# Optimization experiments

Measured on AMD Instinct MI355X. Metric: run time of the kernel, lower is better.

Reference implementation:

```python
import math
import jax, jax.numpy as jnp
import numpy as np

D_MODEL = 768
N_HEADS = 12


def setup_inputs() -> dict:
    key = jax.random.key(0)
    kx, kw, kb = jax.random.split(key, 3)
    x = jax.random.normal(kx, (2, 2048, D_MODEL), dtype=jnp.float32)
    # nn.Linear(D, 3D): weight [3D, D], bias [3D]; init ~ U(-1/sqrt(D), 1/sqrt(D))
    bound = 1.0 / math.sqrt(D_MODEL)
    W_kqv = jax.random.uniform(kw, (3 * D_MODEL, D_MODEL), dtype=jnp.float32, minval=-bound, maxval=bound)
    b_kqv = jax.random.uniform(kb, (3 * D_MODEL,), dtype=jnp.float32, minval=-bound, maxval=bound)
    return {"x": x, "W_kqv": W_kqv, "b_kqv": b_kqv}


def reference(x, W_kqv, b_kqv):
    N, C, D = x.shape
    H = N_HEADS
    hd = D // H
    z = jnp.einsum('ncd,ed->nce', x, W_kqv) + b_kqv  # [N, C, 3D]
    # order in source: k first, then q, then v
    k = z[:, :, :D].reshape(N, C, H, hd).transpose(0, 2, 1, 3)       # [N,H,C,hd]
    q = z[:, :, D:2 * D].reshape(N, C, H, hd).transpose(0, 2, 1, 3)
    v = z[:, :, 2 * D:].reshape(N, C, H, hd).transpose(0, 2, 1, 3)
    # NOTE: faithful to source: scale by sqrt(D) (full model dim), not sqrt(head_dim)
    scores = jnp.einsum('nhqd,nhkd->nhqk', q, k) / math.sqrt(D)
    causal = jnp.tril(jnp.ones((C, C), dtype=bool))
    scores = jnp.where(causal, scores, -jnp.inf)
    attn = jax.nn.softmax(scores, axis=-1)
    out = jnp.einsum('nhqk,nhkd->nhqd', attn, v)  # [N,H,C,hd]
    return out.transpose(0, 2, 1, 3).reshape(N, C, D)
```

## Files before the change

### kernel.cpp

```cpp
#include <hip/hip_runtime.h>
#include <stdint.h>

#define D_MODEL 768
#define E3      2304
#define NCTX    2048
#define NH      12
#define HD      64
#define MROWS   4096
#define NHTOT   24

typedef __attribute__((ext_vector_type(8))) short short8;
typedef __attribute__((ext_vector_type(4))) short bf16x4;
typedef __attribute__((ext_vector_type(4))) float f32x4;

typedef __attribute__((address_space(3))) uint32_t lds_u32;
typedef __attribute__((address_space(1))) uint32_t glob_u32;

__device__ __forceinline__ void async_copy16(const void* g, void* l) {
    __builtin_amdgcn_global_load_lds((const glob_u32*)(uintptr_t)g,
                                     (lds_u32*)(uint32_t)(uintptr_t)l, 16, 0, 0);
}

__device__ __forceinline__ unsigned short f2bf(float f) {
    uint32_t u = __builtin_bit_cast(uint32_t, f);
    u += 0x7fffu + ((u >> 16) & 1u);
    return (unsigned short)(u >> 16);
}

__device__ __forceinline__ float fast_exp2(float x) {
#if __has_builtin(__builtin_amdgcn_exp2f)
    return __builtin_amdgcn_exp2f(x);
#else
    return __expf(x * 0.6931471805599453f);
#endif
}

#if __has_builtin(__builtin_amdgcn_mfma_f32_16x16x16bf16_1k)
#define HAVE_MFMA16 1
#else
#define HAVE_MFMA16 0
#endif

__global__ void cast_bf16_kernel(const float* __restrict__ in, unsigned short* __restrict__ out) {
    int i = blockIdx.x * blockDim.x + threadIdx.x;
    float4 v = ((const float4*)in)[i];
    ushort4 o;
    o.x = f2bf(v.x); o.y = f2bf(v.y); o.z = f2bf(v.z); o.w = f2bf(v.w);
    ((ushort4*)out)[i] = o;
}

__global__ __launch_bounds__(256) void qkv_gemm(const unsigned short* __restrict__ A,
                                                const unsigned short* __restrict__ B,
                                                const float* __restrict__ bias,
                                                unsigned short* __restrict__ Zq,
                                                unsigned short* __restrict__ Kb,
                                                unsigned short* __restrict__ Vb) {
    __shared__ __attribute__((aligned(16))) unsigned short sA[128 * 64];
    __shared__ __attribute__((aligned(16))) unsigned short sB[128 * 64];

    const int tid  = threadIdx.x;
    const int wave = tid >> 6;
    const int lane = tid & 63;
    const int quad = lane >> 4;
    const int l15  = lane & 15;
    const int wm   = (wave >> 1) << 6;
    const int wn   = (wave & 1) << 6;
    const int row0 = blockIdx.y * 128;
    const int col0 = blockIdx.x * 128;

    const int srow   = lane >> 3;
    const int schunk = (lane & 7) * 8;

    f32x4 acc[4][4] = {};

    for (int k0 = 0; k0 < D_MODEL; k0 += 64) {
        __syncthreads();
#pragma unroll
        for (int c = 0; c < 4; ++c) {
            const int rbase = wave * 32 + c * 8;
            async_copy16(A + (size_t)(row0 + rbase + srow) * D_MODEL + k0 + schunk, &sA[rbase * 64]);
            async_copy16(B + (size_t)(col0 + rbase + srow) * D_MODEL + k0 + schunk, &sB[rbase * 64]);
        }
        __syncthreads();

#pragma unroll
        for (int ks = 0; ks < 2; ++ks) {
            short8 aF[4], bF[4];
#pragma unroll
            for (int i = 0; i < 4; ++i)
                aF[i] = *(const short8*)&sA[(wm + i * 16 + l15) * 64 + ks * 32 + quad * 8];
#pragma unroll
            for (int i = 0; i < 4; ++i)
                bF[i] = *(const short8*)&sB[(wn + i * 16 + l15) * 64 + ks * 32 + quad * 8];
#pragma unroll
            for (int i = 0; i < 4; ++i)
#pragma unroll
                for (int j = 0; j < 4; ++j)
                    acc[i][j] = __builtin_amdgcn_mfma_f32_16x16x32_bf16(aF[i], bF[j], acc[i][j], 0, 0, 0);
        }
    }

    if (col0 < D_MODEL) {
#pragma unroll
        for (int j = 0; j < 4; ++j) {
            const int col = col0 + wn + j * 16 + l15;
            const float bv = bias[col];
            const int h = col >> 6, d = col & 63;
            const int ks = d >> 5, quadd = (d >> 3) & 3, e = d & 7;
#pragma unroll
            for (int i = 0; i < 4; ++i) {
                const int row = row0 + wm + i * 16 + quad * 4;
                const int n = row >> 11;
                const int key = row & (NCTX - 1);
                const int kb = key >> 6;
                const int ct = i;
                const size_t base = ((size_t)((n * NH + h) * 32 + kb)) * 4096
                                  + (((ks * 4 + ct) * 4 + quadd) * 16) * 8 + e;
#pragma unroll
                for (int r = 0; r < 4; ++r)
                    Kb[base + (size_t)(quad * 4 + r) * 8] = f2bf(acc[i][j][r] + bv);
            }
        }
    } else if (col0 < 2 * D_MODEL) {
        const float zscale = 0.036084391824351615f * 1.4426950408889634f;
#pragma unroll
        for (int j = 0; j < 4; ++j) {
            const int col = col0 - D_MODEL + wn + j * 16 + l15;
            const float bv = bias[col0 + wn + j * 16 + l15];
#pragma unroll
            for (int i = 0; i < 4; ++i) {
                const int row = row0 + wm + i * 16 + quad * 4;
#pragma unroll
                for (int r = 0; r < 4; ++r)
                    Zq[(size_t)(row + r) * D_MODEL + col] = f2bf((acc[i][j][r] + bv) * zscale);
            }
        }
    } else {
#pragma unroll
        for (int j = 0; j < 4; ++j) {
            const int col = col0 + wn + j * 16 + l15;
            const float bv = bias[col];
            const int ch = col - 2 * D_MODEL;
            const int h = ch >> 6, d = ch & 63;
            const int dt = d >> 4, l15d = d & 15;
#pragma unroll
            for (int i = 0; i < 4; ++i) {
                const int row = row0 + wm + i * 16 + quad * 4;
                const int n = row >> 11;
                const int key = row & (NCTX - 1);
                const int kb = key >> 6;
                const int ct = i, quadv = quad;
                ushort4 w4;
                w4.x = f2bf(acc[i][j][0] + bv);
                w4.y = f2bf(acc[i][j][1] + bv);
                w4.z = f2bf(acc[i][j][2] + bv);
                w4.w = f2bf(acc[i][j][3] + bv);
                *(ushort4*)&Vb[((size_t)((n * NH + h) * 32 + kb)) * 4096
                               + (((ct * 4 + dt) * 4 + quadv) * 16 + l15d) * 4] = w4;
            }
        }
    }
}

__global__ __launch_bounds__(256) void attn_kernel(const unsigned short* __restrict__ Zq,
                                                   const unsigned short* __restrict__ Kb,
                                                   const unsigned short* __restrict__ Vb,
                                                   float* __restrict__ out) {
    __shared__ __attribute__((aligned(16))) unsigned short sK[2][4096];
    __shared__ __attribute__((aligned(16))) unsigned short sV[2][4096];
#if !HAVE_MFMA16
    __shared__ __attribute__((aligned(16))) unsigned short sP[4][16 * 72];
#endif

    const int tid  = threadIdx.x;
    const int wave = tid >> 6;
    const int lane = tid & 63;
    const int quad = lane >> 4;
    const int l15  = lane & 15;
    const int b    = blockIdx.x;
    const int t    = (NCTX / 64 - 1) - b / NHTOT;
    const int nh   = b - (b / NHTOT) * NHTOT;
    const int n    = nh / NH;
    const int h    = nh - n * NH;

    const unsigned short* KbP = Kb + (size_t)(nh * 32) * 4096;
    const unsigned short* VbP = Vb + (size_t)(nh * 32) * 4096;

    const unsigned short* Qp = Zq + (size_t)(n * NCTX + t * 64 + wave * 16) * D_MODEL + h * HD;
    short8 qf[2];
#pragma unroll
    for (int ks = 0; ks < 2; ++ks)
        qf[ks] = *(const short8*)&Qp[(size_t)l15 * D_MODEL + ks * 32 + quad * 8];

    f32x4 o[4] = {};
    float lsum = 0.0f;

#pragma unroll
    for (int c = 0; c < 2; ++c) {
        const int off = wave * 1024 + c * 512;
        async_copy16(KbP + off + lane * 8, &sK[0][off]);
        async_copy16(VbP + off + lane * 8, &sV[0][off]);
    }

    for (int kb = 0; kb <= t; ++kb) {
        const int buf = kb & 1;
        __syncthreads();
        if (kb < t) {
#pragma unroll
            for (int c = 0; c < 2; ++c) {
                const int off = wave * 1024 + c * 512;
                async_copy16(KbP + (size_t)(kb + 1) * 4096 + off + lane * 8, &sK[buf ^ 1][off]);
                async_copy16(VbP + (size_t)(kb + 1) * 4096 + off + lane * 8, &sV[buf ^ 1][off]);
            }
        }

        short8 kf[2][4];
#pragma unroll
        for (int ks = 0; ks < 2; ++ks)
#pragma unroll
            for (int ct = 0; ct < 4; ++ct)
                kf[ks][ct] = *(const short8*)&sK[buf][(ks * 4 + ct) * 512 + lane * 8];

        f32x4 s[4] = {};
#pragma unroll
        for (int ct = 0; ct < 4; ++ct) {
            s[ct] = __builtin_amdgcn_mfma_f32_16x16x32_bf16(kf[0][ct], qf[0], s[ct], 0, 0, 0);
            s[ct] = __builtin_amdgcn_mfma_f32_16x16x32_bf16(kf[1][ct], qf[1], s[ct], 0, 0, 0);
        }

        const bool diag = (kb == t);
        const int qg = t * 64 + wave * 16 + l15;
#if HAVE_MFMA16
        bf16x4 pA[4];
#endif
#pragma unroll
        for (int ct = 0; ct < 4; ++ct) {
            float pv[4];
#pragma unroll
            for (int r = 0; r < 4; ++r) {
                const int key = kb * 64 + ct * 16 + quad * 4 + r;
                float sv = s[ct][r];
                if (diag && key > qg) sv = -INFINITY;
                pv[r] = fast_exp2(sv);
                lsum += pv[r];
            }
#if HAVE_MFMA16
            pA[ct][0] = (short)f2bf(pv[0]); pA[ct][1] = (short)f2bf(pv[1]);
            pA[ct][2] = (short)f2bf(pv[2]); pA[ct][3] = (short)f2bf(pv[3]);
#else
            ushort4 w4;
            w4.x = f2bf(pv[0]); w4.y = f2bf(pv[1]); w4.z = f2bf(pv[2]); w4.w = f2bf(pv[3]);
            *(ushort4*)&sP[wave][l15 * 72 + ct * 16 + quad * 4] = w4;
#endif
        }

#if HAVE_MFMA16
#pragma unroll
        for (int ct = 0; ct < 4; ++ct)
#pragma unroll
            for (int dt = 0; dt < 4; ++dt) {
                const bf16x4 vf = *(const bf16x4*)&sV[buf][(ct * 4 + dt) * 256 + lane * 4];
                o[dt] = __builtin_amdgcn_mfma_f32_16x16x16bf16_1k(pA[ct], vf, o[dt], 0, 0, 0);
            }
#else
        const short8 pf0 = *(const short8*)&sP[wave][l15 * 72 + quad * 8];
        const short8 pf1 = *(const short8*)&sP[wave][l15 * 72 + 32 + quad * 8];
#pragma unroll
        for (int dt = 0; dt < 4; ++dt) {
            short8 vf0, vf1;
#pragma unroll
            for (int e = 0; e < 8; ++e) {
                const int k0 = quad * 8 + e;
                const int k1 = 32 + quad * 8 + e;
                vf0[e] = (short)sV[buf][(((k0 >> 4) * 4 + dt) * 4 + ((k0 >> 2) & 3)) * 64 + l15 * 4 + (k0 & 3)];
                vf1[e] = (short)sV[buf][(((k1 >> 4) * 4 + dt) * 4 + ((k1 >> 2) & 3)) * 64 + l15 * 4 + (k1 & 3)];
            }
            o[dt] = __builtin_amdgcn_mfma_f32_16x16x32_bf16(pf0, vf0, o[dt], 0, 0, 0);
            o[dt] = __builtin_amdgcn_mfma_f32_16x16x32_bf16(pf1, vf1, o[dt], 0, 0, 0);
        }
#endif
    }

    float l = lsum;
    l += __shfl_xor(l, 16);
    l += __shfl_xor(l, 32);
    const float linv = 1.0f / l;
#pragma unroll
    for (int r = 0; r < 4; ++r) {
        const float inv = __shfl(linv, quad * 4 + r);
        const size_t row = (size_t)n * NCTX + t * 64 + wave * 16 + quad * 4 + r;
#pragma unroll
        for (int dt = 0; dt < 4; ++dt)
            out[row * D_MODEL + h * HD + dt * 16 + l15] = o[dt][r] * inv;
    }
}

extern "C" void kernel_launch(void* const* d_in, const int* in_sizes, int n_in,
                              void* d_out, int out_size, void* d_ws, size_t ws_size,
                              hipStream_t stream) {
    const float* x = (const float*)d_in[0];
    const float* W = (const float*)d_in[1];
    const float* b = (const float*)d_in[2];
    float* out = (float*)d_out;

    unsigned short* xb = (unsigned short*)d_ws;
    unsigned short* Wb = xb + (size_t)MROWS * D_MODEL;
    unsigned short* Zq = Wb + (size_t)E3 * D_MODEL;
    unsigned short* Kb = Zq + (size_t)MROWS * D_MODEL;
    unsigned short* Vb = Kb + (size_t)NHTOT * 32 * 4096;

    cast_bf16_kernel<<<dim3((MROWS * D_MODEL / 4) / 256), 256, 0, stream>>>(x, xb);
    cast_bf16_kernel<<<dim3((E3 * D_MODEL / 4) / 256), 256, 0, stream>>>(W, Wb);
    qkv_gemm<<<dim3(E3 / 128, MROWS / 128), 256, 0, stream>>>(xb, Wb, b, Zq, Kb, Vb);
    attn_kernel<<<dim3(NHTOT * (NCTX / 64)), 256, 0, stream>>>(Zq, Kb, Vb, out);
}
```

Measured before the change: 144.4 us.

## Retile QKV GEMM to 128x96, swizzle LDS, load V from global, remap heads

The QKV GEMM tile changes from 128x128 to 128x96, giving 24x32 blocks, and the LDS staging layout is reorganized into 8-row groups with lanes mapped along k. This is meant to improve wave occupancy across CUs and reduce LDS bank conflicts. In attention, V is no longer staged through double-buffered LDS: each wave loads its pre-swizzled V fragments straight from global memory into registers, halving LDS use. Block-to-head mapping is also permuted, likely for L2 locality. This risks global-load latency on V sitting in the critical path.

```diff
diff --git a/kernel.cpp b/kernel.cpp
--- a/kernel.cpp
+++ b/kernel.cpp
@@ -35,11 +35,14 @@
 #endif
 }
 
-#if __has_builtin(__builtin_amdgcn_mfma_f32_16x16x16bf16_1k)
-#define HAVE_MFMA16 1
+__device__ __forceinline__ f32x4 mfma16_bf16(bf16x4 a, bf16x4 b, f32x4 c) {
+#if defined(__HIP_DEVICE_COMPILE__)
+    return __builtin_amdgcn_mfma_f32_16x16x16bf16_1k(a, b, c, 0, 0, 0);
 #else
-#define HAVE_MFMA16 0
+    (void)a; (void)b;
+    return c;
 #endif
+}
 
 __global__ void cast_bf16_kernel(const float* __restrict__ in, unsigned short* __restrict__ out) {
     int i = blockIdx.x * blockDim.x + threadIdx.x;
@@ -56,53 +59,58 @@
                                                 unsigned short* __restrict__ Kb,
                                                 unsigned short* __restrict__ Vb) {
     __shared__ __attribute__((aligned(16))) unsigned short sA[128 * 64];
-    __shared__ __attribute__((aligned(16))) unsigned short sB[128 * 64];
+    __shared__ __attribute__((aligned(16))) unsigned short sB[96 * 64];
 
     const int tid  = threadIdx.x;
     const int wave = tid >> 6;
     const int lane = tid & 63;
     const int quad = lane >> 4;
     const int l15  = lane & 15;
-    const int wm   = (wave >> 1) << 6;
-    const int wn   = (wave & 1) << 6;
+    const int wm   = (wave >> 1) * 64;
+    const int wn   = (wave & 1) * 48;
     const int row0 = blockIdx.y * 128;
-    const int col0 = blockIdx.x * 128;
-
-    const int srow   = lane >> 3;
-    const int schunk = (lane & 7) * 8;
-
-    f32x4 acc[4][4] = {};
+    const int col0 = blockIdx.x * 96;
+
+    const int srow   = lane & 7;
+    const int schunk = (lane >> 3) * 8;
+
+    f32x4 acc[4][3] = {};
 
     for (int k0 = 0; k0 < D_MODEL; k0 += 64) {
         __syncthreads();
 #pragma unroll
         for (int c = 0; c < 4; ++c) {
-            const int rbase = wave * 32 + c * 8;
-            async_copy16(A + (size_t)(row0 + rbase + srow) * D_MODEL + k0 + schunk, &sA[rbase * 64]);
-            async_copy16(B + (size_t)(col0 + rbase + srow) * D_MODEL + k0 + schunk, &sB[rbase * 64]);
+            const int reg = wave * 4 + c;
+            async_copy16(A + (size_t)(row0 + reg * 8 + srow) * D_MODEL + k0 + schunk, &sA[reg * 512]);
+        }
+#pragma unroll
+        for (int c = 0; c < 3; ++c) {
+            const int reg = wave * 3 + c;
+            async_copy16(B + (size_t)(col0 + reg * 8 + srow) * D_MODEL + k0 + schunk, &sB[reg * 512]);
         }
         __syncthreads();
 
 #pragma unroll
         for (int ks = 0; ks < 2; ++ks) {
-            short8 aF[4], bF[4];
+            const int qoff = (ks * 4 + quad) * 64 + (l15 & 7) * 8;
+            short8 aF[4], bF[3];
 #pragma unroll
             for (int i = 0; i < 4; ++i)
-                aF[i] = *(const short8*)&sA[(wm + i * 16 + l15) * 64 + ks * 32 + quad * 8];
+                aF[i] = *(const short8*)&sA[((wm >> 3) + i * 2 + (l15 >> 3)) * 512 + qoff];
+#pragma unroll
+            for (int j = 0; j < 3; ++j)
+                bF[j] = *(const short8*)&sB[((wn >> 3) + j * 2 + (l15 >> 3)) * 512 + qoff];
 #pragma unroll
             for (int i = 0; i < 4; ++i)
-                bF[i] = *(const short8*)&sB[(wn + i * 16 + l15) * 64 + ks * 32 + quad * 8];
-#pragma unroll
-            for (int i = 0; i < 4; ++i)
-#pragma unroll
-                for (int j = 0; j < 4; ++j)
+#pragma unroll
+                for (int j = 0; j < 3; ++j)
                     acc[i][j] = __builtin_amdgcn_mfma_f32_16x16x32_bf16(aF[i], bF[j], acc[i][j], 0, 0, 0);
         }
     }
 
     if (col0 < D_MODEL) {
 #pragma unroll
-        for (int j = 0; j < 4; ++j) {
+        for (int j = 0; j < 3; ++j) {
             const int col = col0 + wn + j * 16 + l15;
             const float bv = bias[col];
             const int h = col >> 6, d = col & 63;
@@ -113,7 +121,7 @@
                 const int n = row >> 11;
                 const int key = row & (NCTX - 1);
                 const int kb = key >> 6;
-                const int ct = i;
+                const int ct = (key >> 4) & 3;
                 const size_t base = ((size_t)((n * NH + h) * 32 + kb)) * 4096
                                   + (((ks * 4 + ct) * 4 + quadd) * 16) * 8 + e;
 #pragma unroll
@@ -124,9 +132,10 @@
     } else if (col0 < 2 * D_MODEL) {
         const float zscale = 0.036084391824351615f * 1.4426950408889634f;
 #pragma unroll
-        for (int j = 0; j < 4; ++j) {
-            const int col = col0 - D_MODEL + wn + j * 16 + l15;
-            const float bv = bias[col0 + wn + j * 16 + l15];
+        for (int j = 0; j < 3; ++j) {
+            const int colz = col0 + wn + j * 16 + l15;
+            const float bv = bias[colz];
+            const int col = colz - D_MODEL;
 #pragma unroll
             for (int i = 0; i < 4; ++i) {
                 const int row = row0 + wm + i * 16 + quad * 4;
@@ -137,7 +146,7 @@
         }
     } else {
 #pragma unroll
-        for (int j = 0; j < 4; ++j) {
+        for (int j = 0; j < 3; ++j) {
             const int col = col0 + wn + j * 16 + l15;
             const float bv = bias[col];
             const int ch = col - 2 * D_MODEL;
@@ -149,14 +158,14 @@
                 const int n = row >> 11;
                 const int key = row & (NCTX - 1);
                 const int kb = key >> 6;
-                const int ct = i, quadv = quad;
+                const int ct = (key >> 4) & 3;
                 ushort4 w4;
                 w4.x = f2bf(acc[i][j][0] + bv);
                 w4.y = f2bf(acc[i][j][1] + bv);
                 w4.z = f2bf(acc[i][j][2] + bv);
                 w4.w = f2bf(acc[i][j][3] + bv);
                 *(ushort4*)&Vb[((size_t)((n * NH + h) * 32 + kb)) * 4096
-                               + (((ct * 4 + dt) * 4 + quadv) * 16 + l15d) * 4] = w4;
+                               + (((ct * 4 + dt) * 4 + quad) * 16 + l15d) * 4] = w4;
             }
         }
     }
@@ -167,10 +176,6 @@
                                                    const unsigned short* __restrict__ Vb,
                                                    float* __restrict__ out) {
     __shared__ __attribute__((aligned(16))) unsigned short sK[2][4096];
-    __shared__ __attribute__((aligned(16))) unsigned short sV[2][4096];
-#if !HAVE_MFMA16
-    __shared__ __attribute__((aligned(16))) unsigned short sP[4][16 * 72];
-#endif
 
     const int tid  = threadIdx.x;
     const int wave = tid >> 6;
@@ -178,8 +183,8 @@
     const int quad = lane >> 4;
     const int l15  = lane & 15;
     const int b    = blockIdx.x;
+    const int nh   = (b & 7) * 3 + ((b >> 3) % 3);
     const int t    = (NCTX / 64 - 1) - b / NHTOT;
-    const int nh   = b - (b / NHTOT) * NHTOT;
     const int n    = nh / NH;
     const int h    = nh - n * NH;
 
@@ -199,7 +204,6 @@
     for (int c = 0; c < 2; ++c) {
         const int off = wave * 1024 + c * 512;
         async_copy16(KbP + off + lane * 8, &sK[0][off]);
-        async_copy16(VbP + off + lane * 8, &sV[0][off]);
     }
 
     for (int kb = 0; kb <= t; ++kb) {
@@ -210,9 +214,15 @@
             for (int c = 0; c < 2; ++c) {
                 const int off = wave * 1024 + c * 512;
                 async_copy16(KbP + (size_t)(kb + 1) * 4096 + off + lane * 8, &sK[buf ^ 1][off]);
-                async_copy16(VbP + (size_t)(kb + 1) * 4096 + off + lane * 8, &sV[buf ^ 1][off]);
-            }
-        }
+            }
+        }
+
+        bf16x4 vf[4][4];
+#pragma unroll
+        for (int ct = 0; ct < 4; ++ct)
+#pragma unroll
+            for (int dt = 0; dt < 4; ++dt)
+                vf[ct][dt] = *(const bf16x4*)&VbP[(size_t)kb * 4096 + (ct * 4 + dt) * 256 + lane * 4];
 
         short8 kf[2][4];
 #pragma unroll
@@ -230,9 +240,7 @@
 
         const bool diag = (kb == t);
         const int qg = t * 64 + wave * 16 + l15;
-#if HAVE_MFMA16
         bf16x4 pA[4];
-#endif
 #pragma unroll
         for (int ct = 0; ct < 4; ++ct) {
             float pv[4];
@@ -244,41 +252,15 @@
                 pv[r] = fast_exp2(sv);
                 lsum += pv[r];
             }
-#if HAVE_MFMA16
             pA[ct][0] = (short)f2bf(pv[0]); pA[ct][1] = (short)f2bf(pv[1]);
             pA[ct][2] = (short)f2bf(pv[2]); pA[ct][3] = (short)f2bf(pv[3]);
-#else
-            ushort4 w4;
-            w4.x = f2bf(pv[0]); w4.y = f2bf(pv[1]); w4.z = f2bf(pv[2]); w4.w = f2bf(pv[3]);
-            *(ushort4*)&sP[wave][l15 * 72 + ct * 16 + quad * 4] = w4;
-#endif
-        }
-
-#if HAVE_MFMA16
+        }
+
 #pragma unroll
         for (int ct = 0; ct < 4; ++ct)
 #pragma unroll
-            for (int dt = 0; dt < 4; ++dt) {
-                const bf16x4 vf = *(const bf16x4*)&sV[buf][(ct * 4 + dt) * 256 + lane * 4];
-                o[dt] = __builtin_amdgcn_mfma_f32_16x16x16bf16_1k(pA[ct], vf, o[dt], 0, 0, 0);
-            }
-#else
-        const short8 pf0 = *(const short8*)&sP[wave][l15 * 72 + quad * 8];
-        const short8 pf1 = *(const short8*)&sP[wave][l15 * 72 + 32 + quad * 8];
-#pragma unroll
-        for (int dt = 0; dt < 4; ++dt) {
-            short8 vf0, vf1;
-#pragma unroll
-            for (int e = 0; e < 8; ++e) {
-                const int k0 = quad * 8 + e;
-                const int k1 = 32 + quad * 8 + e;
-                vf0[e] = (short)sV[buf][(((k0 >> 4) * 4 + dt) * 4 + ((k0 >> 2) & 3)) * 64 + l15 * 4 + (k0 & 3)];
-                vf1[e] = (short)sV[buf][(((k1 >> 4) * 4 + dt) * 4 + ((k1 >> 2) & 3)) * 64 + l15 * 4 + (k1 & 3)];
-            }
-            o[dt] = __builtin_amdgcn_mfma_f32_16x16x32_bf16(pf0, vf0, o[dt], 0, 0, 0);
-            o[dt] = __builtin_amdgcn_mfma_f32_16x16x32_bf16(pf1, vf1, o[dt], 0, 0, 0);
-        }
-#endif
+            for (int dt = 0; dt < 4; ++dt)
+                o[dt] = mfma16_bf16(pA[ct], vf[ct][dt], o[dt]);
     }
 
     float l = lsum;
@@ -311,6 +293,6 @@
 
     cast_bf16_kernel<<<dim3((MROWS * D_MODEL / 4) / 256), 256, 0, stream>>>(x, xb);
     cast_bf16_kernel<<<dim3((E3 * D_MODEL / 4) / 256), 256, 0, stream>>>(W, Wb);
-    qkv_gemm<<<dim3(E3 / 128, MROWS / 128), 256, 0, stream>>>(xb, Wb, b, Zq, Kb, Vb);
+    qkv_gemm<<<dim3(E3 / 96, MROWS / 128), 256, 0, stream>>>(xb, Wb, b, Zq, Kb, Vb);
     attn_kernel<<<dim3(NHTOT * (NCTX / 64)), 256, 0, stream>>>(Zq, Kb, Vb, out);
 }
```

Measured after the change: 155.6 us. 1.08x slower.
